# Kernel tuning notes

Measured on AMD Instinct MI355X. Metric: run time of the kernel, lower is better.

## Reference

```python
import jax, jax.numpy as jnp
import numpy as np

D_MODEL = 1024
H = 16
D_K = D_MODEL // H  # 64
RANK = 5
ALPHA = 1.0


def _lora_linear(x, W, b, dW, dB):
    # merged weight: W + alpha * dB @ dW  (shape [out, in]); F.linear -> x @ W_merged.T + b
    Wm = W + ALPHA * (dB @ dW)
    return x @ Wm.T + b


def setup_inputs() -> dict:
    key = jax.random.key(0)
    ks = jax.random.split(key, 16)
    b_s, nq = 2, 2048
    s = 1.0 / np.sqrt(D_MODEL).astype(np.float32)
    inp = {
        "x": jax.random.normal(ks[0], (b_s, nq, D_MODEL), dtype=jnp.float32),
    }
    names = ["q", "k", "v", "o"]
    i = 1
    for n in names:
        inp[f"{n}_w"] = jax.random.normal(ks[i], (D_MODEL, D_MODEL), dtype=jnp.float32) * s; i += 1
        inp[f"{n}_b"] = jnp.zeros((D_MODEL,), dtype=jnp.float32)
        inp[f"{n}_dw"] = jax.random.normal(ks[i], (RANK, D_MODEL), dtype=jnp.float32) * 0.01; i += 1
        inp[f"{n}_db"] = jax.random.normal(ks[i], (D_MODEL, RANK), dtype=jnp.float32) * 0.01; i += 1
    return inp


def reference(x, q_w, q_b, q_dw, q_db, k_w, k_b, k_dw, k_db,
              v_w, v_b, v_dw, v_db, o_w, o_b, o_dw, o_db):
    b_s, nq, _ = x.shape
    q = _lora_linear(x, q_w, q_b, q_dw, q_db).reshape(b_s, nq, H, D_K)
    k = _lora_linear(x, k_w, k_b, k_dw, k_db).reshape(b_s, nq, H, D_K)
    v = _lora_linear(x, v_w, v_b, v_dw, v_db).reshape(b_s, nq, H, D_K)
    # scores: [b, h, q, k]
    att = jnp.einsum("bqhd,bkhd->bhqk", q, k) / np.sqrt(D_K).astype(np.float32)
    att = jax.nn.softmax(att, axis=-1)
    out = jnp.einsum("bhqk,bkhd->bqhd", att, v).reshape(b_s, nq, H * D_K)
    out = _lora_linear(out, o_w, o_b, o_dw, o_db)
    return out
```

## Files before the change

kernel.cpp:

```cpp
#include <hip/hip_runtime.h>
#include <hip/hip_bf16.h>

#define NQ 2048
#define NB 2

typedef unsigned short u16;
typedef unsigned int u32;
typedef _Float16 f16;
typedef __attribute__((ext_vector_type(8))) _Float16 half8;
typedef __attribute__((ext_vector_type(2))) __fp16 fp16x2;
typedef __attribute__((ext_vector_type(4))) float f32x4;
typedef __attribute__((ext_vector_type(2))) unsigned int u32x2;

#define MFMAH(A, B, C) __builtin_amdgcn_mfma_f32_16x16x32_f16(A, B, C, 0, 0, 0)

__device__ __forceinline__ u16 f2h(float x) {
    f16 h = (f16)x;
    return *(u16*)&h;
}
__device__ __forceinline__ u32 pk_h2(float a, float b) {
    union { fp16x2 v; u32 u; } c;
    c.v = __builtin_amdgcn_cvt_pkrtz(a, b);
    return c.u;
}
__device__ __forceinline__ float fexp2(float x) {
#if __has_builtin(__builtin_amdgcn_exp2f)
    return __builtin_amdgcn_exp2f(x);
#else
    return exp2f(x);
#endif
}
__device__ __forceinline__ void glds16(const u16* g, u16* l) {
    typedef const __attribute__((address_space(1))) u16 gu16;
    typedef __attribute__((address_space(3))) u16 lu16;
    __builtin_amdgcn_global_load_lds((gu16*)g, (lu16*)l, 16, 0, 0);
}
template <int N> __device__ __forceinline__ void waitvm() {
    if constexpr (N == 0) asm volatile("s_waitcnt vmcnt(0)" ::: "memory");
    else if constexpr (N == 3) asm volatile("s_waitcnt vmcnt(3)" ::: "memory");
    else if constexpr (N == 4) asm volatile("s_waitcnt vmcnt(4)" ::: "memory");
    else static_assert(N == 0 || N == 3 || N == 4, "add vmcnt case");
}
__device__ __forceinline__ void pl32swap(u32& a, u32& b) {
#if __has_builtin(__builtin_amdgcn_permlane32_swap)
    u32x2 r = __builtin_amdgcn_permlane32_swap(a, b, false, false);
    a = r[0]; b = r[1];
#else
    asm volatile("v_permlane32_swap_b32 %0, %1" : "+v"(a), "+v"(b));
#endif
}
__device__ __forceinline__ void pl16swap(u32& a, u32& b) {
#if __has_builtin(__builtin_amdgcn_permlane16_swap)
    u32x2 r = __builtin_amdgcn_permlane16_swap(a, b, false, false);
    a = r[0]; b = r[1];
#else
    asm volatile("v_permlane16_swap_b32 %0, %1" : "+v"(a), "+v"(b));
#endif
}

#define QSCALE 0.18033688011112042f

__global__ __launch_bounds__(256) void prep(
    const float* __restrict__ w0, const float* __restrict__ dw0, const float* __restrict__ db0,
    const float* __restrict__ w1, const float* __restrict__ dw1, const float* __restrict__ db1,
    const float* __restrict__ w2, const float* __restrict__ dw2, const float* __restrict__ db2,
    const float* __restrict__ w3, const float* __restrict__ dw3, const float* __restrict__ db3,
    u16* __restrict__ Wf,
    const float* __restrict__ x, u16* __restrict__ xf,
    const float* __restrict__ b0, const float* __restrict__ b1,
    const float* __restrict__ b2, const float* __restrict__ b3,
    float* __restrict__ ball) {
    const int bid = blockIdx.x;
    if (bid >= 8192) {
        int t = (bid - 8192) * 256 + threadIdx.x;
        int which = t >> 10;
        const float* B = (which == 0) ? b0 : (which == 1) ? b1 : (which == 2) ? b2 : b3;
        float v = B[t & 1023];
        if (which == 0) v *= QSCALE;
        ball[t] = v;
        return;
    }
    if (bid >= 4096) {
        int i4 = ((bid - 4096) * 256 + threadIdx.x) * 4;
        float4 v = *(const float4*)&x[i4];
        *(uint2*)&xf[i4] = make_uint2(pk_h2(v.x, v.y), pk_h2(v.z, v.w));
        return;
    }
    int i4 = (bid * 256 + threadIdx.x) * 4;
    int row = i4 >> 10, col = i4 & 1023;
    int which = row >> 10, lr = row & 1023;
    const float* W  = (which == 0) ? w0  : (which == 1) ? w1  : (which == 2) ? w2  : w3;
    const float* dW = (which == 0) ? dw0 : (which == 1) ? dw1 : (which == 2) ? dw2 : dw3;
    const float* dB = (which == 0) ? db0 : (which == 1) ? db1 : (which == 2) ? db2 : db3;
    float4 acc = *(const float4*)&W[lr * 1024 + col];
#pragma unroll
    for (int r = 0; r < 5; ++r) {
        float s = dB[lr * 5 + r];
        float4 w4 = *(const float4*)&dW[r * 1024 + col];
        acc.x += s * w4.x; acc.y += s * w4.y;
        acc.z += s * w4.z; acc.w += s * w4.w;
    }
    if (which == 0) { acc.x *= QSCALE; acc.y *= QSCALE; acc.z *= QSCALE; acc.w *= QSCALE; }
    ushort4 o = make_ushort4(f2h(acc.x), f2h(acc.y), f2h(acc.z), f2h(acc.w));
    *(ushort4*)&Wf[i4] = o;
}

template <int TM>
__global__ __launch_bounds__(256) void gemm_f16(
    const u16* __restrict__ Af, const u16* __restrict__ Bf,
    const float* __restrict__ bias,
    float* __restrict__ Cf, u16* __restrict__ Cb, int ldc,
    u16* __restrict__ VtOut) {
    constexpr int MI = TM / 32;
    constexpr int LPS = TM / 64 + 2;
    __shared__ u16 As[3][TM * 32];
    __shared__ u16 Bs[3][128 * 32];
    const int tid = threadIdx.x;
    const int wid = tid >> 6, lane = tid & 63;
    const int ln = lane & 15, quad = lane >> 4;
    const int bm = blockIdx.y * TM, bn = blockIdx.x * 128;
    const int wm = (wid >> 1) * (TM / 2), wn = (wid & 1) * 64;
    const int lrow = lane >> 2;
    const int schunk = ((lane & 3) ^ ((lrow >> 1) & 3)) * 8;
    const int kswz = (quad ^ ((ln >> 1) & 3)) * 8;

    f32x4 acc[MI][4];
#pragma unroll
    for (int i = 0; i < MI; ++i)
#pragma unroll
        for (int j = 0; j < 4; ++j) acc[i][j] = (f32x4){0.f, 0.f, 0.f, 0.f};

    auto GSTAGE = [&](int s, int bu) {
#pragma unroll
        for (int p = 0; p < TM / 64; ++p) {
            int r = p * 64 + wid * 16;
            glds16(&Af[(bm + r + lrow) * 1024 + s * 32 + schunk], &As[bu][r * 32]);
        }
#pragma unroll
        for (int p = 0; p < 2; ++p) {
            int r = p * 64 + wid * 16;
            glds16(&Bf[(bn + r + lrow) * 1024 + s * 32 + schunk], &Bs[bu][r * 32]);
        }
    };

    auto COMPUTE = [&](int bu) {
        half8 a[MI], b[4];
#pragma unroll
        for (int j = 0; j < 4; ++j)
            b[j] = *(const half8*)&Bs[bu][(wn + j * 16 + ln) * 32 + kswz];
#pragma unroll
        for (int i = 0; i < MI; ++i)
            a[i] = *(const half8*)&As[bu][(wm + i * 16 + ln) * 32 + kswz];
#pragma unroll
        for (int i = 0; i < MI; ++i)
#pragma unroll
            for (int j = 0; j < 4; ++j)
                acc[i][j] = MFMAH(a[i], b[j], acc[i][j]);
    };

    GSTAGE(0, 0);
    GSTAGE(1, 1);
    waitvm<LPS>();
    __syncthreads();

    for (int s = 0; s < 30; s += 3) {
        GSTAGE(s + 2, 2); COMPUTE(0); waitvm<LPS>(); __syncthreads();
        GSTAGE(s + 3, 0); COMPUTE(1); waitvm<LPS>(); __syncthreads();
        GSTAGE(s + 4, 1); COMPUTE(2); waitvm<LPS>(); __syncthreads();
    }
    COMPUTE(0);
    waitvm<0>();
    __syncthreads();
    COMPUTE(1);

    if (VtOut && bn >= 2048) {
#pragma unroll
        for (int i = 0; i < MI; ++i)
#pragma unroll
            for (int j = 0; j < 4; ++j) {
                int col = bn + wn + j * 16 + ln;
                float bv = bias[col];
                int colV = col - 2048;
                int row0 = bm + wm + i * 16 + quad * 4;
                ushort4 pk = make_ushort4(f2h(acc[i][j][0] + bv), f2h(acc[i][j][1] + bv),
                                          f2h(acc[i][j][2] + bv), f2h(acc[i][j][3] + bv));
                *(ushort4*)&VtOut[colV * 4096 + row0] = pk;
            }
        return;
    }

#pragma unroll
    for (int i = 0; i < MI; ++i)
#pragma unroll
        for (int j = 0; j < 4; ++j) {
            int col = bn + wn + j * 16 + ln;
            float bv = bias[col];
#pragma unroll
            for (int r = 0; r < 4; ++r) {
                int row = bm + wm + i * 16 + quad * 4 + r;
                float v = acc[i][j][r] + bv;
                if (Cb) Cb[row * ldc + col] = f2h(v);
                else    Cf[row * ldc + col] = v;
            }
        }
}

__global__ __launch_bounds__(256) void flash_f16(
    const u16* __restrict__ QKV, const u16* __restrict__ Vt,
    u16* __restrict__ AO) {
    __shared__ u16 Ks[2][2][64 * 32];
    __shared__ u16 Vs[2][2][64 * 32];

    const int tid = threadIdx.x;
    const int wid = tid >> 6, lane = tid & 63;
    const int ln = lane & 15, quad = lane >> 4;
    const int qt = blockIdx.x, h = blockIdx.y, b = blockIdx.z;
    const int rowbase = b * NQ;
    const int col0 = h * 64;
    const int q0 = rowbase + qt * 128 + wid * 32;
    const int lrow = lane >> 2;
    const int kchunk = ((lane & 3) ^ ((lrow >> 1) & 3)) * 8;
    const int kswz = (quad ^ ((ln >> 1) & 3)) * 8;

    const half8 ones = {(f16)1, (f16)1, (f16)1, (f16)1,
                        (f16)1, (f16)1, (f16)1, (f16)1};

    half8 qf[2][2];
#pragma unroll
    for (int mi = 0; mi < 2; ++mi)
#pragma unroll
        for (int kc = 0; kc < 2; ++kc)
            qf[mi][kc] = *(const half8*)&QKV[(q0 + mi * 16 + ln) * 3072 + col0 +
                                             kc * 32 + quad * 8];

    f32x4 accO[4][2];
    f32x4 accS[2];
#pragma unroll
    for (int mi = 0; mi < 2; ++mi) {
        accS[mi] = (f32x4){0.f, 0.f, 0.f, 0.f};
#pragma unroll
        for (int a = 0; a < 4; ++a) accO[a][mi] = (f32x4){0.f, 0.f, 0.f, 0.f};
    }

    const int NT = NQ / 64;
    const u16* Kg = QKV + (rowbase + wid * 16 + lrow) * 3072 + 1024 + col0 + kchunk;
    const u16* Vg = Vt + (col0 + wid * 16 + lrow) * 4096 + rowbase + kchunk;

#define STAGEK(kt2, bu)                                        \
    {                                                          \
        const u16* kg_ = Kg + (kt2) * (64 * 3072);             \
        glds16(kg_,      &Ks[bu][0][wid * 512]);               \
        glds16(kg_ + 32, &Ks[bu][1][wid * 512]);               \
    }
#define STAGEV(kt2, bu)                                        \
    {                                                          \
        const u16* vg_ = Vg + (kt2) * 64;                      \
        glds16(vg_,      &Vs[bu][0][wid * 512]);               \
        glds16(vg_ + 32, &Vs[bu][1][wid * 512]);               \
    }

    auto qk_exp = [&](int kb, half8 (&pf)[2][2]) {
        f32x4 s[4][2];
#pragma unroll
        for (int a = 0; a < 4; ++a) {
            half8 kf0 = *(const half8*)&Ks[kb][0][(a * 16 + ln) * 32 + kswz];
            half8 kf1 = *(const half8*)&Ks[kb][1][(a * 16 + ln) * 32 + kswz];
#pragma unroll
            for (int mi = 0; mi < 2; ++mi) {
                f32x4 t = (f32x4){0.f, 0.f, 0.f, 0.f};
                t = MFMAH(kf0, qf[mi][0], t);
                t = MFMAH(kf1, qf[mi][1], t);
                s[a][mi] = t;
            }
        }
#pragma unroll
        for (int mi = 0; mi < 2; ++mi)
#pragma unroll
            for (int kc = 0; kc < 2; ++kc) {
                u32 c0 = pk_h2(fexp2(s[2 * kc][mi][0]), fexp2(s[2 * kc][mi][1]));
                u32 c1 = pk_h2(fexp2(s[2 * kc][mi][2]), fexp2(s[2 * kc][mi][3]));
                u32 c2 = pk_h2(fexp2(s[2 * kc + 1][mi][0]), fexp2(s[2 * kc + 1][mi][1]));
                u32 c3 = pk_h2(fexp2(s[2 * kc + 1][mi][2]), fexp2(s[2 * kc + 1][mi][3]));
                pl32swap(c0, c2);
                pl32swap(c1, c3);
                pl16swap(c0, c2);
                pl16swap(c1, c3);
                union { u32 u[4]; half8 h; } pu;
                pu.u[0] = c0; pu.u[1] = c1; pu.u[2] = c2; pu.u[3] = c3;
                pf[mi][kc] = pu.h;
                accS[mi] = MFMAH(ones, pf[mi][kc], accS[mi]);
            }
    };

    auto pv = [&](const half8 (&pf)[2][2], int vb) {
#pragma unroll
        for (int a = 0; a < 4; ++a) {
            half8 vf0 = *(const half8*)&Vs[vb][0][(a * 16 + ln) * 32 + kswz];
            half8 vf1 = *(const half8*)&Vs[vb][1][(a * 16 + ln) * 32 + kswz];
#pragma unroll
            for (int mi = 0; mi < 2; ++mi) {
                accO[a][mi] = MFMAH(vf0, pf[mi][0], accO[a][mi]);
                accO[a][mi] = MFMAH(vf1, pf[mi][1], accO[a][mi]);
            }
        }
    };

    half8 pfA[2][2], pfB[2][2];

    STAGEK(0, 0);
    STAGEV(0, 0);
    asm volatile("s_waitcnt vmcnt(0)" ::: "memory");
    __syncthreads();
    STAGEK(1, 1);
    qk_exp(0, pfA);
    asm volatile("s_waitcnt vmcnt(0)" ::: "memory");
    __syncthreads();

    for (int kt = 0; kt < NT - 2; kt += 2) {
        STAGEK(kt + 2, 0);
        STAGEV(kt + 1, 1);
        qk_exp(1, pfB);
        pv(pfA, 0);
        asm volatile("s_waitcnt vmcnt(0)" ::: "memory");
        __syncthreads();

        STAGEK(kt + 3, 1);
        STAGEV(kt + 2, 0);
        qk_exp(0, pfA);
        pv(pfB, 1);
        asm volatile("s_waitcnt vmcnt(0)" ::: "memory");
        __syncthreads();
    }
    STAGEV(NT - 1, 1);
    qk_exp(1, pfB);
    pv(pfA, 0);
    asm volatile("s_waitcnt vmcnt(0)" ::: "memory");
    __syncthreads();
    pv(pfB, 1);
#undef STAGEK
#undef STAGEV

#pragma unroll
    for (int mi = 0; mi < 2; ++mi) {
        float inv = 1.f / accS[mi][0];
        int q = q0 + mi * 16 + ln;
#pragma unroll
        for (int a = 0; a < 4; ++a) {
            ushort4 pk = make_ushort4(f2h(accO[a][mi][0] * inv),
                                      f2h(accO[a][mi][1] * inv),
                                      f2h(accO[a][mi][2] * inv),
                                      f2h(accO[a][mi][3] * inv));
            *(ushort4*)&AO[q * 1024 + col0 + a * 16 + quad * 4] = pk;
        }
    }
}

extern "C" void kernel_launch(void* const* d_in, const int* in_sizes, int n_in,
                              void* d_out, int out_size, void* d_ws, size_t ws_size,
                              hipStream_t stream) {
    const float* x = (const float*)d_in[0];
    const float* w[4]  = {(const float*)d_in[1],  (const float*)d_in[5],
                          (const float*)d_in[9],  (const float*)d_in[13]};
    const float* bv[4] = {(const float*)d_in[2],  (const float*)d_in[6],
                          (const float*)d_in[10], (const float*)d_in[14]};
    const float* dw[4] = {(const float*)d_in[3],  (const float*)d_in[7],
                          (const float*)d_in[11], (const float*)d_in[15]};
    const float* db[4] = {(const float*)d_in[4],  (const float*)d_in[8],
                          (const float*)d_in[12], (const float*)d_in[16]};

    u16* p = (u16*)d_ws;
    u16* Wf  = p; p += 4096 * 1024;
    u16* xf  = p; p += 4096 * 1024;
    u16* QKV = p; p += 4096 * 3072;
    u16* Vt  = p; p += 1024 * 4096;
    float* ball = (float*)p;
    u16* AO = xf;

    prep<<<8208, 256, 0, stream>>>(w[0], dw[0], db[0], w[1], dw[1], db[1],
                                   w[2], dw[2], db[2], w[3], dw[3], db[3], Wf,
                                   x, xf,
                                   bv[0], bv[1], bv[2], bv[3], ball);

    gemm_f16<128><<<dim3(24, 32), 256, 0, stream>>>(xf, Wf, ball,
                                                    nullptr, QKV, 3072, Vt);

    flash_f16<<<dim3(NQ / 128, 16, NB), 256, 0, stream>>>(QKV, Vt, AO);

    gemm_f16<64><<<dim3(8, 64), 256, 0, stream>>>(AO, Wf + 3072 * 1024,
                                                  ball + 3072, (float*)d_out, nullptr, 1024,
                                                  nullptr);
}
```

Before: 217.7 us.

## Double flash-attention KV tile to 128 keys and raise MFMA wave priority

Grows the key/value tile each pipeline stage processes from 64 to 128 keys. This halves the number of loop iterations, and with them the barriers and waitcnt stalls per query block. The QK/exp step is split into two halves over the larger tile. s_setprio is raised around the MFMA sections so matrix work is favoured over other waves. In exchange, LDS use doubles and the P fragments take more registers, which may reduce occupancy.

Result: faster. 212.6 us (-2.4%).

```diff
diff --git a/kernel.cpp b/kernel.cpp
--- a/kernel.cpp
+++ b/kernel.cpp
@@ -208,8 +208,8 @@
 __global__ __launch_bounds__(256) void flash_f16(
     const u16* __restrict__ QKV, const u16* __restrict__ Vt,
     u16* __restrict__ AO) {
-    __shared__ u16 Ks[2][2][64 * 32];
-    __shared__ u16 Vs[2][2][64 * 32];
+    __shared__ u16 Ks[2][2][128 * 32];
+    __shared__ u16 Vs[2][4][64 * 32];
 
     const int tid = threadIdx.x;
     const int wid = tid >> 6, lane = tid & 63;
@@ -242,27 +242,33 @@
         for (int a = 0; a < 4; ++a) accO[a][mi] = (f32x4){0.f, 0.f, 0.f, 0.f};
     }
 
-    const int NT = NQ / 64;
-    const u16* Kg = QKV + (rowbase + wid * 16 + lrow) * 3072 + 1024 + col0 + kchunk;
+    const int NT = NQ / 128;
+    const u16* Kg = QKV + (rowbase + wid * 32 + lrow) * 3072 + 1024 + col0 + kchunk;
     const u16* Vg = Vt + (col0 + wid * 16 + lrow) * 4096 + rowbase + kchunk;
 
-#define STAGEK(kt2, bu)                                        \
-    {                                                          \
-        const u16* kg_ = Kg + (kt2) * (64 * 3072);             \
-        glds16(kg_,      &Ks[bu][0][wid * 512]);               \
-        glds16(kg_ + 32, &Ks[bu][1][wid * 512]);               \
+#define STAGEK(kt2, bu)                                              \
+    {                                                                \
+        const u16* kg_ = Kg + (kt2) * (128 * 3072);                  \
+        glds16(kg_,              &Ks[bu][0][wid * 1024]);            \
+        glds16(kg_ + 32,         &Ks[bu][1][wid * 1024]);            \
+        glds16(kg_ + 16 * 3072,      &Ks[bu][0][wid * 1024 + 512]);  \
+        glds16(kg_ + 16 * 3072 + 32, &Ks[bu][1][wid * 1024 + 512]);  \
     }
 #define STAGEV(kt2, bu)                                        \
     {                                                          \
-        const u16* vg_ = Vg + (kt2) * 64;                      \
+        const u16* vg_ = Vg + (kt2) * 128;                     \
         glds16(vg_,      &Vs[bu][0][wid * 512]);               \
         glds16(vg_ + 32, &Vs[bu][1][wid * 512]);               \
-    }
-
-    auto qk_exp = [&](int kb, half8 (&pf)[2][2]) {
+        glds16(vg_ + 64, &Vs[bu][2][wid * 512]);               \
+        glds16(vg_ + 96, &Vs[bu][3][wid * 512]);               \
+    }
+
+    auto qk_half = [&](int kb, int ah, half8 (&pf)[2][4]) {
         f32x4 s[4][2];
-#pragma unroll
-        for (int a = 0; a < 4; ++a) {
+        __builtin_amdgcn_s_setprio(1);
+#pragma unroll
+        for (int a4 = 0; a4 < 4; ++a4) {
+            int a = ah * 4 + a4;
             half8 kf0 = *(const half8*)&Ks[kb][0][(a * 16 + ln) * 32 + kswz];
             half8 kf1 = *(const half8*)&Ks[kb][1][(a * 16 + ln) * 32 + kswz];
 #pragma unroll
@@ -270,69 +276,80 @@
                 f32x4 t = (f32x4){0.f, 0.f, 0.f, 0.f};
                 t = MFMAH(kf0, qf[mi][0], t);
                 t = MFMAH(kf1, qf[mi][1], t);
-                s[a][mi] = t;
+                s[a4][mi] = t;
             }
         }
+        __builtin_amdgcn_s_setprio(0);
 #pragma unroll
         for (int mi = 0; mi < 2; ++mi)
 #pragma unroll
-            for (int kc = 0; kc < 2; ++kc) {
-                u32 c0 = pk_h2(fexp2(s[2 * kc][mi][0]), fexp2(s[2 * kc][mi][1]));
-                u32 c1 = pk_h2(fexp2(s[2 * kc][mi][2]), fexp2(s[2 * kc][mi][3]));
-                u32 c2 = pk_h2(fexp2(s[2 * kc + 1][mi][0]), fexp2(s[2 * kc + 1][mi][1]));
-                u32 c3 = pk_h2(fexp2(s[2 * kc + 1][mi][2]), fexp2(s[2 * kc + 1][mi][3]));
+            for (int kc2 = 0; kc2 < 2; ++kc2) {
+                u32 c0 = pk_h2(fexp2(s[2 * kc2][mi][0]), fexp2(s[2 * kc2][mi][1]));
+                u32 c1 = pk_h2(fexp2(s[2 * kc2][mi][2]), fexp2(s[2 * kc2][mi][3]));
+                u32 c2 = pk_h2(fexp2(s[2 * kc2 + 1][mi][0]), fexp2(s[2 * kc2 + 1][mi][1]));
+                u32 c3 = pk_h2(fexp2(s[2 * kc2 + 1][mi][2]), fexp2(s[2 * kc2 + 1][mi][3]));
                 pl32swap(c0, c2);
                 pl32swap(c1, c3);
                 pl16swap(c0, c2);
                 pl16swap(c1, c3);
                 union { u32 u[4]; half8 h; } pu;
                 pu.u[0] = c0; pu.u[1] = c1; pu.u[2] = c2; pu.u[3] = c3;
-                pf[mi][kc] = pu.h;
-                accS[mi] = MFMAH(ones, pf[mi][kc], accS[mi]);
+                pf[mi][ah * 2 + kc2] = pu.h;
+                accS[mi] = MFMAH(ones, pf[mi][ah * 2 + kc2], accS[mi]);
             }
     };
 
-    auto pv = [&](const half8 (&pf)[2][2], int vb) {
+    auto pv = [&](const half8 (&pf)[2][4], int vb) {
+        __builtin_amdgcn_s_setprio(1);
 #pragma unroll
         for (int a = 0; a < 4; ++a) {
             half8 vf0 = *(const half8*)&Vs[vb][0][(a * 16 + ln) * 32 + kswz];
             half8 vf1 = *(const half8*)&Vs[vb][1][(a * 16 + ln) * 32 + kswz];
+            half8 vf2 = *(const half8*)&Vs[vb][2][(a * 16 + ln) * 32 + kswz];
+            half8 vf3 = *(const half8*)&Vs[vb][3][(a * 16 + ln) * 32 + kswz];
 #pragma unroll
             for (int mi = 0; mi < 2; ++mi) {
                 accO[a][mi] = MFMAH(vf0, pf[mi][0], accO[a][mi]);
                 accO[a][mi] = MFMAH(vf1, pf[mi][1], accO[a][mi]);
+                accO[a][mi] = MFMAH(vf2, pf[mi][2], accO[a][mi]);
+                accO[a][mi] = MFMAH(vf3, pf[mi][3], accO[a][mi]);
             }
         }
+        __builtin_amdgcn_s_setprio(0);
     };
 
-    half8 pfA[2][2], pfB[2][2];
+    half8 pfA[2][4], pfB[2][4];
 
     STAGEK(0, 0);
     STAGEV(0, 0);
     asm volatile("s_waitcnt vmcnt(0)" ::: "memory");
     __syncthreads();
     STAGEK(1, 1);
-    qk_exp(0, pfA);
+    qk_half(0, 0, pfA);
+    qk_half(0, 1, pfA);
     asm volatile("s_waitcnt vmcnt(0)" ::: "memory");
     __syncthreads();
 
     for (int kt = 0; kt < NT - 2; kt += 2) {
         STAGEK(kt + 2, 0);
         STAGEV(kt + 1, 1);
-        qk_exp(1, pfB);
+        qk_half(1, 0, pfB);
+        qk_half(1, 1, pfB);
         pv(pfA, 0);
         asm volatile("s_waitcnt vmcnt(0)" ::: "memory");
         __syncthreads();
 
         STAGEK(kt + 3, 1);
         STAGEV(kt + 2, 0);
-        qk_exp(0, pfA);
+        qk_half(0, 0, pfA);
+        qk_half(0, 1, pfA);
         pv(pfB, 1);
         asm volatile("s_waitcnt vmcnt(0)" ::: "memory");
         __syncthreads();
     }
     STAGEV(NT - 1, 1);
-    qk_exp(1, pfB);
+    qk_half(1, 0, pfB);
+    qk_half(1, 1, pfB);
     pv(pfA, 0);
     asm volatile("s_waitcnt vmcnt(0)" ::: "memory");
     __syncthreads();
```

## Triple-buffer K/V LDS tiles with partial vmcnt waits and MFMA priority

Applied to the files above, without the earlier changes.

Grows the flash-attention K and V shared-memory buffers from two stages to three and prefetches tiles further ahead. Waits now use partial vmcnt counts instead of draining every global-to-LDS load before each barrier, and the loop is unrolled by six to rotate buffers. It also raises wave priority with s_setprio around the MFMA sections. The goal is to hide global load latency better, at the cost of more LDS per block (possible occupancy loss) and one redundant clamped tail load.

New measurement: 214.1 us. No clear change (-1.6%).

```diff
diff --git a/kernel.cpp b/kernel.cpp
--- a/kernel.cpp
+++ b/kernel.cpp
@@ -37,9 +37,11 @@
 }
 template <int N> __device__ __forceinline__ void waitvm() {
     if constexpr (N == 0) asm volatile("s_waitcnt vmcnt(0)" ::: "memory");
+    else if constexpr (N == 2) asm volatile("s_waitcnt vmcnt(2)" ::: "memory");
     else if constexpr (N == 3) asm volatile("s_waitcnt vmcnt(3)" ::: "memory");
     else if constexpr (N == 4) asm volatile("s_waitcnt vmcnt(4)" ::: "memory");
-    else static_assert(N == 0 || N == 3 || N == 4, "add vmcnt case");
+    else if constexpr (N == 6) asm volatile("s_waitcnt vmcnt(6)" ::: "memory");
+    else static_assert(N == 0 || N == 2 || N == 3 || N == 4 || N == 6, "add case");
 }
 __device__ __forceinline__ void pl32swap(u32& a, u32& b) {
 #if __has_builtin(__builtin_amdgcn_permlane32_swap)
@@ -208,8 +210,8 @@
 __global__ __launch_bounds__(256) void flash_f16(
     const u16* __restrict__ QKV, const u16* __restrict__ Vt,
     u16* __restrict__ AO) {
-    __shared__ u16 Ks[2][2][64 * 32];
-    __shared__ u16 Vs[2][2][64 * 32];
+    __shared__ u16 Ks[3][2][64 * 32];
+    __shared__ u16 Vs[3][2][64 * 32];
 
     const int tid = threadIdx.x;
     const int wid = tid >> 6, lane = tid & 63;
@@ -242,7 +244,6 @@
         for (int a = 0; a < 4; ++a) accO[a][mi] = (f32x4){0.f, 0.f, 0.f, 0.f};
     }
 
-    const int NT = NQ / 64;
     const u16* Kg = QKV + (rowbase + wid * 16 + lrow) * 3072 + 1024 + col0 + kchunk;
     const u16* Vg = Vt + (col0 + wid * 16 + lrow) * 4096 + rowbase + kchunk;
 
@@ -261,6 +262,7 @@
 
     auto qk_exp = [&](int kb, half8 (&pf)[2][2]) {
         f32x4 s[4][2];
+        __builtin_amdgcn_s_setprio(1);
 #pragma unroll
         for (int a = 0; a < 4; ++a) {
             half8 kf0 = *(const half8*)&Ks[kb][0][(a * 16 + ln) * 32 + kswz];
@@ -273,6 +275,7 @@
                 s[a][mi] = t;
             }
         }
+        __builtin_amdgcn_s_setprio(0);
 #pragma unroll
         for (int mi = 0; mi < 2; ++mi)
 #pragma unroll
@@ -293,6 +296,7 @@
     };
 
     auto pv = [&](const half8 (&pf)[2][2], int vb) {
+        __builtin_amdgcn_s_setprio(1);
 #pragma unroll
         for (int a = 0; a < 4; ++a) {
             half8 vf0 = *(const half8*)&Vs[vb][0][(a * 16 + ln) * 32 + kswz];
@@ -303,38 +307,48 @@
                 accO[a][mi] = MFMAH(vf1, pf[mi][1], accO[a][mi]);
             }
         }
+        __builtin_amdgcn_s_setprio(0);
     };
 
     half8 pfA[2][2], pfB[2][2];
 
-    STAGEK(0, 0);
-    STAGEV(0, 0);
-    asm volatile("s_waitcnt vmcnt(0)" ::: "memory");
+    STAGEK(0, 0); STAGEV(0, 0);
+    STAGEK(1, 1); STAGEV(1, 1);
+    STAGEK(2, 2);
+    waitvm<6>();
     __syncthreads();
-    STAGEK(1, 1);
     qk_exp(0, pfA);
-    asm volatile("s_waitcnt vmcnt(0)" ::: "memory");
+    waitvm<2>();
     __syncthreads();
 
-    for (int kt = 0; kt < NT - 2; kt += 2) {
-        STAGEK(kt + 2, 0);
-        STAGEV(kt + 1, 1);
-        qk_exp(1, pfB);
-        pv(pfA, 0);
-        asm volatile("s_waitcnt vmcnt(0)" ::: "memory");
-        __syncthreads();
-
-        STAGEK(kt + 3, 1);
-        STAGEV(kt + 2, 0);
-        qk_exp(0, pfA);
-        pv(pfB, 1);
-        asm volatile("s_waitcnt vmcnt(0)" ::: "memory");
-        __syncthreads();
-    }
-    STAGEV(NT - 1, 1);
+    for (int kt = 0; kt < 30; kt += 6) {
+        STAGEK(kt + 3, 0); STAGEV(kt + 2, 2);
+        qk_exp(1, pfB); pv(pfA, 0);
+        waitvm<4>(); __syncthreads();
+
+        STAGEK(kt + 4, 1); STAGEV(kt + 3, 0);
+        qk_exp(2, pfA); pv(pfB, 1);
+        waitvm<4>(); __syncthreads();
+
+        STAGEK(kt + 5, 2); STAGEV(kt + 4, 1);
+        qk_exp(0, pfB); pv(pfA, 2);
+        waitvm<4>(); __syncthreads();
+
+        STAGEK(kt + 6, 0); STAGEV(kt + 5, 2);
+        qk_exp(1, pfA); pv(pfB, 0);
+        waitvm<4>(); __syncthreads();
+
+        STAGEK(kt + 7, 1); STAGEV(kt + 6, 0);
+        qk_exp(2, pfB); pv(pfA, 1);
+        waitvm<4>(); __syncthreads();
+
+        STAGEK(((kt + 8) > 31 ? 31 : (kt + 8)), 2); STAGEV(kt + 7, 1);
+        qk_exp(0, pfA); pv(pfB, 2);
+        waitvm<4>(); __syncthreads();
+    }
     qk_exp(1, pfB);
     pv(pfA, 0);
-    asm volatile("s_waitcnt vmcnt(0)" ::: "memory");
+    waitvm<0>();
     __syncthreads();
     pv(pfB, 1);
 #undef STAGEK
```

## Split attention keys across two blocks and merge partial outputs in a combine kernel

Applied to the files above, without the earlier changes.

The flash attention kernel now splits the key range into two halves, launching twice as many blocks. Each half writes its normalised partial output plus its softmax row sum. The second half's output goes into the unused V columns of QKV and the sums go into the freed weight buffer. A new combine kernel reweights the two partials by their sums to form the final attention output. This aims to raise occupancy and CU utilisation, at the cost of an extra launch and extra global traffic. It also adds s_setprio around the MFMA sections.

Measured after the change: 222.4 us. 1.02x slower.

```diff
diff --git a/kernel.cpp b/kernel.cpp
--- a/kernel.cpp
+++ b/kernel.cpp
@@ -18,6 +18,10 @@
     f16 h = (f16)x;
     return *(u16*)&h;
 }
+__device__ __forceinline__ float h2f(u16 u) {
+    f16 h = *(f16*)&u;
+    return (float)h;
+}
 __device__ __forceinline__ u32 pk_h2(float a, float b) {
     union { fp16x2 v; u32 u; } c;
     c.v = __builtin_amdgcn_cvt_pkrtz(a, b);
@@ -39,7 +43,7 @@
     if constexpr (N == 0) asm volatile("s_waitcnt vmcnt(0)" ::: "memory");
     else if constexpr (N == 3) asm volatile("s_waitcnt vmcnt(3)" ::: "memory");
     else if constexpr (N == 4) asm volatile("s_waitcnt vmcnt(4)" ::: "memory");
-    else static_assert(N == 0 || N == 3 || N == 4, "add vmcnt case");
+    else static_assert(N == 0 || N == 3 || N == 4, "add case");
 }
 __device__ __forceinline__ void pl32swap(u32& a, u32& b) {
 #if __has_builtin(__builtin_amdgcn_permlane32_swap)
@@ -207,15 +211,17 @@
 
 __global__ __launch_bounds__(256) void flash_f16(
     const u16* __restrict__ QKV, const u16* __restrict__ Vt,
-    u16* __restrict__ AO) {
+    u16* __restrict__ P1, u16* __restrict__ AO, float* __restrict__ svec) {
     __shared__ u16 Ks[2][2][64 * 32];
     __shared__ u16 Vs[2][2][64 * 32];
 
     const int tid = threadIdx.x;
     const int wid = tid >> 6, lane = tid & 63;
     const int ln = lane & 15, quad = lane >> 4;
-    const int qt = blockIdx.x, h = blockIdx.y, b = blockIdx.z;
+    const int qt = blockIdx.x, h = blockIdx.y;
+    const int b = blockIdx.z >> 1, hb = blockIdx.z & 1;
     const int rowbase = b * NQ;
+    const int keybase = hb * (NQ / 2);
     const int col0 = h * 64;
     const int q0 = rowbase + qt * 128 + wid * 32;
     const int lrow = lane >> 2;
@@ -242,9 +248,10 @@
         for (int a = 0; a < 4; ++a) accO[a][mi] = (f32x4){0.f, 0.f, 0.f, 0.f};
     }
 
-    const int NT = NQ / 64;
-    const u16* Kg = QKV + (rowbase + wid * 16 + lrow) * 3072 + 1024 + col0 + kchunk;
-    const u16* Vg = Vt + (col0 + wid * 16 + lrow) * 4096 + rowbase + kchunk;
+    const int NT = (NQ / 2) / 64;
+    const u16* Kg = QKV + (rowbase + keybase + wid * 16 + lrow) * 3072 + 1024 +
+                    col0 + kchunk;
+    const u16* Vg = Vt + (col0 + wid * 16 + lrow) * 4096 + rowbase + keybase + kchunk;
 
 #define STAGEK(kt2, bu)                                        \
     {                                                          \
@@ -261,6 +268,7 @@
 
     auto qk_exp = [&](int kb, half8 (&pf)[2][2]) {
         f32x4 s[4][2];
+        __builtin_amdgcn_s_setprio(1);
 #pragma unroll
         for (int a = 0; a < 4; ++a) {
             half8 kf0 = *(const half8*)&Ks[kb][0][(a * 16 + ln) * 32 + kswz];
@@ -273,6 +281,7 @@
                 s[a][mi] = t;
             }
         }
+        __builtin_amdgcn_s_setprio(0);
 #pragma unroll
         for (int mi = 0; mi < 2; ++mi)
 #pragma unroll
@@ -293,6 +302,7 @@
     };
 
     auto pv = [&](const half8 (&pf)[2][2], int vb) {
+        __builtin_amdgcn_s_setprio(1);
 #pragma unroll
         for (int a = 0; a < 4; ++a) {
             half8 vf0 = *(const half8*)&Vs[vb][0][(a * 16 + ln) * 32 + kswz];
@@ -303,6 +313,7 @@
                 accO[a][mi] = MFMAH(vf1, pf[mi][1], accO[a][mi]);
             }
         }
+        __builtin_amdgcn_s_setprio(0);
     };
 
     half8 pfA[2][2], pfB[2][2];
@@ -340,19 +351,41 @@
 #undef STAGEK
 #undef STAGEV
 
+    u16* dst = hb ? (P1 + 2048) : AO;
+    const int ldd = hb ? 3072 : 1024;
 #pragma unroll
     for (int mi = 0; mi < 2; ++mi) {
         float inv = 1.f / accS[mi][0];
         int q = q0 + mi * 16 + ln;
+        if (quad == 0) svec[((hb * 4096 + q) << 4) + h] = accS[mi][0];
 #pragma unroll
         for (int a = 0; a < 4; ++a) {
             ushort4 pk = make_ushort4(f2h(accO[a][mi][0] * inv),
                                       f2h(accO[a][mi][1] * inv),
                                       f2h(accO[a][mi][2] * inv),
                                       f2h(accO[a][mi][3] * inv));
-            *(ushort4*)&AO[q * 1024 + col0 + a * 16 + quad * 4] = pk;
-        }
-    }
+            *(ushort4*)&dst[(size_t)q * ldd + col0 + a * 16 + quad * 4] = pk;
+        }
+    }
+}
+
+__global__ __launch_bounds__(256) void combine(
+    const u16* __restrict__ QKV, const float* __restrict__ svec,
+    u16* __restrict__ AO) {
+    const int q = blockIdx.x;
+    const int c = threadIdx.x * 4;
+    const int hh = c >> 6;
+    const float s0 = svec[(q << 4) + hh];
+    const float s1 = svec[((4096 + q) << 4) + hh];
+    const float r = 1.f / (s0 + s1);
+    const float w0 = s0 * r, w1 = s1 * r;
+    ushort4 a0 = *(const ushort4*)&AO[(size_t)q * 1024 + c];
+    ushort4 a1 = *(const ushort4*)&QKV[(size_t)q * 3072 + 2048 + c];
+    ushort4 pk = make_ushort4(f2h(h2f(a0.x) * w0 + h2f(a1.x) * w1),
+                              f2h(h2f(a0.y) * w0 + h2f(a1.y) * w1),
+                              f2h(h2f(a0.z) * w0 + h2f(a1.z) * w1),
+                              f2h(h2f(a0.w) * w0 + h2f(a1.w) * w1));
+    *(ushort4*)&AO[(size_t)q * 1024 + c] = pk;
 }
 
 extern "C" void kernel_launch(void* const* d_in, const int* in_sizes, int n_in,
@@ -375,6 +408,7 @@
     u16* Vt  = p; p += 1024 * 4096;
     float* ball = (float*)p;
     u16* AO = xf;
+    float* svec = (float*)Wf;
 
     prep<<<8208, 256, 0, stream>>>(w[0], dw[0], db[0], w[1], dw[1], db[1],
                                    w[2], dw[2], db[2], w[3], dw[3], db[3], Wf,
@@ -384,7 +418,8 @@
     gemm_f16<128><<<dim3(24, 32), 256, 0, stream>>>(xf, Wf, ball,
                                                     nullptr, QKV, 3072, Vt);
 
-    flash_f16<<<dim3(NQ / 128, 16, NB), 256, 0, stream>>>(QKV, Vt, AO);
+    flash_f16<<<dim3(NQ / 128, 16, NB * 2), 256, 0, stream>>>(QKV, Vt, QKV, AO, svec);
+    combine<<<4096, 256, 0, stream>>>(QKV, svec, AO);
 
     gemm_f16<64><<<dim3(8, 64), 256, 0, stream>>>(AO, Wf + 3072 * 1024,
                                                   ball + 3072, (float*)d_out, nullptr, 1024,
```
